# Optimization experiments

Measured on AMD Instinct MI355X. Metric: run time of the kernel, lower is better.

## Reference

```python
import jax, jax.numpy as jnp
import numpy as np

N_EMBD = 1024
N_HEADS = 16
HEAD_DIM = N_EMBD // N_HEADS


def setup_inputs() -> dict:
    key = jax.random.key(0)
    k0, k1, k2, k3, k4 = jax.random.split(key, 5)
    scale = 1.0 / np.sqrt(N_EMBD)
    x = jax.random.normal(k0, (2, 2048, N_EMBD), dtype=jnp.float32)
    # nn.Linear(n_embd, 3*n_embd): weight [3d, d], bias [3d]
    w_qkv = jax.random.normal(k1, (3 * N_EMBD, N_EMBD), dtype=jnp.float32) * scale
    b_qkv = jax.random.normal(k2, (3 * N_EMBD,), dtype=jnp.float32) * scale
    w_proj = jax.random.normal(k3, (N_EMBD, N_EMBD), dtype=jnp.float32) * scale
    b_proj = jax.random.normal(k4, (N_EMBD,), dtype=jnp.float32) * scale
    return {"x": x, "w_qkv": w_qkv, "b_qkv": b_qkv, "w_proj": w_proj, "b_proj": b_proj}


def reference(x, w_qkv, b_qkv, w_proj, b_proj):
    b, l, d = x.shape
    h, f = N_HEADS, HEAD_DIM
    qkv = x @ w_qkv.T + b_qkv                      # [b, l, 3d]
    # rearrange 'b l (c h f) -> c b h l f'
    qkv = qkv.reshape(b, l, 3, h, f)
    q = jnp.transpose(qkv[:, :, 0], (0, 2, 1, 3))  # [b, h, l, f]
    k = jnp.transpose(qkv[:, :, 1], (0, 2, 1, 3))
    v = jnp.transpose(qkv[:, :, 2], (0, 2, 1, 3))
    scores = jnp.einsum('bhqf,bhkf->bhqk', q, k) / jnp.sqrt(jnp.float32(f))
    att = jax.nn.softmax(scores, axis=-1)          # [b, h, l, l]
    y = jnp.einsum('bhqk,bhkf->bhqf', att, v)      # [b, h, l, f]
    y = jnp.transpose(y, (0, 2, 1, 3)).reshape(b, l, d)  # 'b h l f -> b l (h f)'
    return y @ w_proj.T + b_proj
```

## Files before the change

kernel.cpp:

```cpp
#include <hip/hip_runtime.h>
#include <hip/hip_bf16.h>
#include <stdint.h>


typedef unsigned short u16;
typedef __attribute__((ext_vector_type(8))) short short8;
typedef __attribute__((ext_vector_type(4))) float f32x4;
typedef __attribute__((ext_vector_type(16))) float f32x16;
typedef __attribute__((ext_vector_type(4))) unsigned int u32x4;

#define MFMA16(a, b, c) __builtin_amdgcn_mfma_f32_16x16x32_bf16((a), (b), (c), 0, 0, 0)
#define MFMA32(a, b, c) __builtin_amdgcn_mfma_f32_32x32x16_bf16((a), (b), (c), 0, 0, 0)

__device__ __forceinline__ u16 f2bf(float x) {
  union { float f; uint32_t u; } v; v.f = x;
  uint32_t r = v.u + 0x7FFFu + ((v.u >> 16) & 1u);
  return (u16)(r >> 16);
}

__device__ __forceinline__ float fexp2(float x) {
#if __has_builtin(__builtin_amdgcn_exp2f)
  return __builtin_amdgcn_exp2f(x);
#else
  return exp2f(x);
#endif
}

__device__ __forceinline__ uint32_t pkbf(float lo, float hi) {
  uint32_t a = __builtin_bit_cast(uint32_t, lo) + 0x8000u;
  uint32_t b = __builtin_bit_cast(uint32_t, hi) + 0x8000u;
  return __builtin_amdgcn_perm(b, a, 0x07060302u);
}

__device__ __forceinline__ void gload16(const void* g, void* l) {
  __builtin_amdgcn_global_load_lds((const __attribute__((address_space(1))) void*)g,
                                   (__attribute__((address_space(3))) void*)l, 16, 0, 0);
}

__global__ __launch_bounds__(256) void cvt_all(const float* __restrict__ x,
                                               const float* __restrict__ wq,
                                               const float* __restrict__ wp,
                                               u16* __restrict__ xb,
                                               u16* __restrict__ wqb,
                                               u16* __restrict__ wpb) {
  int i = blockIdx.x * 256 + threadIdx.x;
  const float* s; u16* d; int off;
  if (i < 1048576) { s = x; d = xb; off = i; }
  else if (i < 1835008) { s = wq; d = wqb; off = i - 1048576; }
  else { s = wp; d = wpb; off = i - 1835008; }
  float4 f = reinterpret_cast<const float4*>(s)[off];
  ushort4 o;
  o.x = f2bf(f.x); o.y = f2bf(f.y); o.z = f2bf(f.z); o.w = f2bf(f.w);
  reinterpret_cast<ushort4*>(d)[off] = o;
}

template <int EPI>
__global__ __launch_bounds__(256, 4) void gemm_bt(const u16* __restrict__ A,
                                                  const u16* __restrict__ B,
                                                  const float* __restrict__ bias,
                                                  u16* __restrict__ outb,
                                                  float* __restrict__ outf,
                                                  int M, int N, int K) {
  __shared__ u16 smem[16384];
  const int tid = threadIdx.x;
  const int lane = tid & 63;
  const int wid = tid >> 6;
  const int bn = blockIdx.x, bm = blockIdx.y;
  const int row0 = bm * 128, col0 = bn * 128;
  const int wr = wid >> 1, wc = wid & 1;
  const int fr = lane & 15, fq = lane >> 4;

  f32x4 acc[4][4];
  #pragma unroll
  for (int m = 0; m < 4; m++)
    #pragma unroll
    for (int n = 0; n < 4; n++)
      #pragma unroll
      for (int j = 0; j < 4; j++) acc[m][n][j] = 0.f;

  const int cB = tid + 256;
  const int rA1 = tid >> 2, rA2 = cB >> 2;
  const int lA1 = (tid & 3) ^ ((tid >> 3) & 3);
  const int lA2 = (cB & 3) ^ ((cB >> 3) & 3);
  const size_t ga1 = (size_t)rA1 * K + lA1 * 8;
  const size_t ga2 = (size_t)rA2 * K + lA2 * 8;
  const int d1 = tid * 8, d2 = cB * 8;
  const u16* Ab = A + (size_t)row0 * K;
  const u16* Bb = B + (size_t)col0 * K;

  const int sl = (fq ^ ((fr >> 1) & 3)) * 8;

  const int niter = K >> 5;

  {
    u16* s = smem;
    gload16(Ab + ga1, s + d1);
    gload16(Ab + ga2, s + d2);
    gload16(Bb + ga1, s + 4096 + d1);
    gload16(Bb + ga2, s + 4096 + d2);
  }
  __syncthreads();

  for (int t = 0; t < niter; t++) {
    if (t + 1 < niter) {
      u16* s = smem + ((t + 1) & 1) * 8192;
      const size_t k0 = (size_t)(t + 1) * 32;
      gload16(Ab + ga1 + k0, s + d1);
      gload16(Ab + ga2 + k0, s + d2);
      gload16(Bb + ga1 + k0, s + 4096 + d1);
      gload16(Bb + ga2 + k0, s + 4096 + d2);
    }
    const u16* sa = smem + (t & 1) * 8192;
    const u16* sb = sa + 4096;
    short8 a[4], b[4];
    #pragma unroll
    for (int m = 0; m < 4; m++)
      a[m] = *(const short8*)&sa[(wr * 64 + m * 16 + fr) * 32 + sl];
    #pragma unroll
    for (int n = 0; n < 4; n++)
      b[n] = *(const short8*)&sb[(wc * 64 + n * 16 + fr) * 32 + sl];
    __builtin_amdgcn_s_setprio(1);
    #pragma unroll
    for (int m = 0; m < 4; m++)
      #pragma unroll
      for (int n = 0; n < 4; n++)
        acc[m][n] = MFMA16(a[m], b[n], acc[m][n]);
    __builtin_amdgcn_s_setprio(0);
    __syncthreads();
  }

  if (EPI == 0) {
    if (bn < 16) {
      #pragma unroll
      for (int m = 0; m < 4; m++) {
        #pragma unroll
        for (int n = 0; n < 4; n++) {
          #pragma unroll
          for (int j = 0; j < 4; j++) {
            int r = row0 + wr * 64 + m * 16 + fq * 4 + j;
            int c = col0 + wc * 64 + n * 16 + fr;
            float v = acc[m][n][j] + bias[c];
            int d = c & 1023, h = d >> 6, f = d & 63;
            int bb = r >> 11, ll = r & 2047;
            int bhh = bb * 16 + h;
            if (bn < 8) {
              outb[((size_t)bhh * 2048 + ll) * 64 + f] = f2bf(v * 0.18033688f);
            } else {
              outb[4194304u + ((size_t)bhh * 2048 + ll) * 64 + f] = f2bf(v);
            }
          }
        }
      }
    } else {
      u16* sC = smem;
      #pragma unroll
      for (int m = 0; m < 4; m++) {
        #pragma unroll
        for (int n = 0; n < 4; n++) {
          int c_local = wc * 64 + n * 16 + fr;
          int r_base = wr * 64 + m * 16 + fq * 4;
          float bi = bias[col0 + c_local];
          uint2 w;
          w.x = pkbf(acc[m][n][0] + bi, acc[m][n][1] + bi);
          w.y = pkbf(acc[m][n][2] + bi, acc[m][n][3] + bi);
          *(uint2*)&sC[c_local * 128 + (r_base ^ ((c_local & 7) << 3))] = w;
        }
      }
      __syncthreads();
      const int h0 = (col0 - 2048) >> 6;
      const int ll0 = row0 & 2047;
      const int bb = row0 >> 11;
      #pragma unroll
      for (int it = 0; it < 8; it++) {
        int chunk = tid + it * 256;
        int row_c = chunk >> 4, off = chunk & 15;
        short8 v = *(const short8*)&sC[row_c * 128 + ((off * 8) ^ ((row_c & 7) << 3))];
        int h = h0 + (row_c >> 6), f = row_c & 63;
        *(short8*)&outb[8388608u + ((size_t)((bb * 16 + h) * 64 + f)) * 2048 + ll0 + off * 8] = v;
      }
    }
  } else {
    #pragma unroll
    for (int m = 0; m < 4; m++)
      #pragma unroll
      for (int n = 0; n < 4; n++)
        #pragma unroll
        for (int j = 0; j < 4; j++) {
          int r = row0 + wr * 64 + m * 16 + fq * 4 + j;
          int c = col0 + wc * 64 + n * 16 + fr;
          outf[(size_t)r * N + c] = acc[m][n][j] + bias[c];
        }
  }
}

__device__ __forceinline__ void softpack(const f32x16& st, float& lp,
                                         short8& paA, short8& paB) {
  float e[16];
  #pragma unroll
  for (int r = 0; r < 16; r++) e[r] = fexp2(st[r]);
  #pragma unroll
  for (int r = 0; r < 16; r++) lp += e[r];
  #pragma unroll
  for (int cc = 0; cc < 2; cc++) {
    uint32_t g0 = pkbf(e[8 * cc + 0], e[8 * cc + 1]);
    uint32_t g1 = pkbf(e[8 * cc + 2], e[8 * cc + 3]);
    uint32_t g2 = pkbf(e[8 * cc + 4], e[8 * cc + 5]);
    uint32_t g3 = pkbf(e[8 * cc + 6], e[8 * cc + 7]);
    asm volatile("v_permlane32_swap_b32 %0, %1" : "+v"(g0), "+v"(g2));
    asm volatile("v_permlane32_swap_b32 %0, %1" : "+v"(g1), "+v"(g3));
    u32x4 t;
    t[0] = g0; t[1] = g1; t[2] = g2; t[3] = g3;
    if (cc == 0) paA = __builtin_bit_cast(short8, t);
    else paB = __builtin_bit_cast(short8, t);
  }
}

__global__ __launch_bounds__(128, 2) void attn_kernel(const u16* __restrict__ qg,
                                                      const u16* __restrict__ kg,
                                                      const u16* __restrict__ vtg,
                                                      u16* __restrict__ y) {
  __shared__ u16 sK[2][4096];
  __shared__ u16 sVt[2][4096];
  __shared__ float sLv[2][32];
  const int x = blockIdx.x;
  const int bh = (x & 7) * 4 + (x >> 8);
  const int qt = (x >> 3) & 31;
  const int tid = threadIdx.x, l = tid & 63, wid = tid >> 6;
  const int col = l & 31, hi = l >> 5;
  const size_t base = (size_t)bh * 131072;
  const u16* qp = qg + base;
  const u16* kp = kg + base;
  const u16* vp = vtg + base;
  const int qrow = qt * 64 + wid * 32;

  short8 qf[4];
  #pragma unroll
  for (int kk = 0; kk < 4; kk++)
    qf[kk] = *(const short8*)&qp[(size_t)(qrow + col) * 64 + kk * 16 + hi * 8];

  int koff[4], voff[4], dst[4];
  #pragma unroll
  for (int j = 0; j < 4; j++) {
    int c = tid + j * 128;
    int row = c >> 3, slot = c & 7;
    int swc = (slot * 8) ^ ((row & 7) << 3);
    koff[j] = row * 64 + swc;
    voff[j] = row * 2048 + swc;
    dst[j] = c * 8;
  }

  f32x16 o0, o1;
  float lp = 0.f;
  #pragma unroll
  for (int r = 0; r < 16; r++) { o0[r] = 0.f; o1[r] = 0.f; }

  const int rsw = (col & 7) << 3;

  #pragma unroll
  for (int j = 0; j < 4; j++) {
    gload16(kp + koff[j], &sK[0][dst[j]]);
    gload16(vp + voff[j], &sVt[0][dst[j]]);
  }

  int sel = 0;
  for (int t0 = 0; t0 < 2048; t0 += 64) {
    __syncthreads();
    if (t0 + 64 < 2048) {
      const int tn = t0 + 64;
      #pragma unroll
      for (int j = 0; j < 4; j++) {
        gload16(kp + (size_t)tn * 64 + koff[j], &sK[sel ^ 1][dst[j]]);
        gload16(vp + tn + voff[j], &sVt[sel ^ 1][dst[j]]);
      }
    }
    const u16* Kt = sK[sel];
    const u16* Vt = sVt[sel];

    f32x16 st0, st1;
    #pragma unroll
    for (int r = 0; r < 16; r++) { st0[r] = 0.f; st1[r] = 0.f; }
    __builtin_amdgcn_s_setprio(1);
    #pragma unroll
    for (int kk = 0; kk < 4; kk++) {
      short8 kb0 = *(const short8*)&Kt[(col) * 64 + ((kk * 16 + hi * 8) ^ rsw)];
      short8 kb1 = *(const short8*)&Kt[(32 + col) * 64 + ((kk * 16 + hi * 8) ^ rsw)];
      st0 = MFMA32(kb0, qf[kk], st0);
      st1 = MFMA32(kb1, qf[kk], st1);
    }
    __builtin_amdgcn_s_setprio(0);

    short8 pa[4];
    softpack(st0, lp, pa[0], pa[1]);
    softpack(st1, lp, pa[2], pa[3]);

    __builtin_amdgcn_s_setprio(1);
    #pragma unroll
    for (int c = 0; c < 4; c++) {
      short8 vb0 = *(const short8*)&Vt[(col) * 64 + ((c * 16 + hi * 8) ^ rsw)];
      short8 vb1 = *(const short8*)&Vt[(32 + col) * 64 + ((c * 16 + hi * 8) ^ rsw)];
      o0 = MFMA32(pa[c], vb0, o0);
      o1 = MFMA32(pa[c], vb1, o1);
    }
    __builtin_amdgcn_s_setprio(0);
    sel ^= 1;
  }

  float lsum = lp + __shfl_xor(lp, 32);
  float linv = 1.0f / lsum;
  if (l < 32) sLv[wid][col] = linv;
  const int b = bh >> 4, hh = bh & 15;
  #pragma unroll
  for (int fvt = 0; fvt < 2; fvt++) {
    #pragma unroll
    for (int r = 0; r < 16; r++) {
      int q = (r & 3) + 8 * (r >> 2) + 4 * hi;
      float li = sLv[wid][q];
      float v = (fvt == 0 ? o0[r] : o1[r]) * li;
      y[((size_t)(b * 2048 + qrow + q)) * 1024 + hh * 64 + fvt * 32 + col] = f2bf(v);
    }
  }
}

extern "C" void kernel_launch(void* const* d_in, const int* in_sizes, int n_in,
                              void* d_out, int out_size, void* d_ws, size_t ws_size,
                              hipStream_t stream) {
  const float* x = (const float*)d_in[0];
  const float* w_qkv = (const float*)d_in[1];
  const float* b_qkv = (const float*)d_in[2];
  const float* w_proj = (const float*)d_in[3];
  const float* b_proj = (const float*)d_in[4];
  float* out = (float*)d_out;

  u16* ws = (u16*)d_ws;
  u16* xb = ws;
  u16* wq = xb + 4194304;
  u16* wp = wq + 3145728;
  u16* qb = wp + 1048576;
  u16* kb = qb + 4194304;
  u16* vb = kb + 4194304;
  u16* yb = vb + 4194304;

  cvt_all<<<8192, 256, 0, stream>>>(x, w_qkv, w_proj, xb, wq, wp);

  gemm_bt<0><<<dim3(24, 32), 256, 0, stream>>>(xb, wq, b_qkv, qb, nullptr, 4096, 3072, 1024);

  attn_kernel<<<1024, 128, 0, stream>>>(qb, kb, vb, yb);

  gemm_bt<1><<<dim3(8, 32), 256, 0, stream>>>(yb, wp, b_proj, nullptr, out, 4096, 1024, 1024);
}
```

Before: 121.2 us.

## Split attention key range across two wave pairs and merge partial outputs

The attention block grows from 2 to 4 waves. Each pair of waves handles half of the key/value sequence (split-K), with 32-key tiles staged per half. The partial outputs and row sums are then combined through shared memory before normalisation and the store. This raises parallelism and latency hiding per block, at the cost of a shared-memory reduction step and extra synchronisation. It relies on scores needing no max subtraction, same as the existing code.

Result: no change. 121.8 us (+0.4%).

```diff
diff --git a/kernel.cpp b/kernel.cpp
--- a/kernel.cpp
+++ b/kernel.cpp
@@ -89,7 +89,6 @@
   const u16* Bb = B + (size_t)col0 * K;
 
   const int sl = (fq ^ ((fr >> 1) & 3)) * 8;
-
   const int niter = K >> 5;
 
   {
@@ -193,8 +192,8 @@
   }
 }
 
-__device__ __forceinline__ void softpack(const f32x16& st, float& lp,
-                                         short8& paA, short8& paB) {
+__device__ __forceinline__ void softpack1(const f32x16& st, float& lp,
+                                          short8& paA, short8& paB) {
   float e[16];
   #pragma unroll
   for (int r = 0; r < 16; r++) e[r] = fexp2(st[r]);
@@ -215,89 +214,90 @@
   }
 }
 
-__global__ __launch_bounds__(128, 2) void attn_kernel(const u16* __restrict__ qg,
+__global__ __launch_bounds__(256, 4) void attn_kernel(const u16* __restrict__ qg,
                                                       const u16* __restrict__ kg,
                                                       const u16* __restrict__ vtg,
                                                       u16* __restrict__ y) {
-  __shared__ u16 sK[2][4096];
-  __shared__ u16 sVt[2][4096];
-  __shared__ float sLv[2][32];
+  __shared__ u16 sStage[16384];
+  __shared__ float sL2[64];
   const int x = blockIdx.x;
   const int bh = (x & 7) * 4 + (x >> 8);
   const int qt = (x >> 3) & 31;
   const int tid = threadIdx.x, l = tid & 63, wid = tid >> 6;
+  const int qs = wid & 1, kh = wid >> 1;
   const int col = l & 31, hi = l >> 5;
   const size_t base = (size_t)bh * 131072;
   const u16* qp = qg + base;
-  const u16* kp = kg + base;
-  const u16* vp = vtg + base;
-  const int qrow = qt * 64 + wid * 32;
+  const u16* kp = kg + base + (size_t)kh * 1024 * 64;
+  const u16* vp = vtg + base + (size_t)kh * 1024;
+  const int qrow = qt * 64 + qs * 32;
 
   short8 qf[4];
   #pragma unroll
   for (int kk = 0; kk < 4; kk++)
     qf[kk] = *(const short8*)&qp[(size_t)(qrow + col) * 64 + kk * 16 + hi * 8];
 
-  int koff[4], voff[4], dst[4];
-  #pragma unroll
-  for (int j = 0; j < 4; j++) {
-    int c = tid + j * 128;
-    int row = c >> 3, slot = c & 7;
-    int swc = (slot * 8) ^ ((row & 7) << 3);
-    koff[j] = row * 64 + swc;
-    voff[j] = row * 2048 + swc;
-    dst[j] = c * 8;
-  }
+  const int kc_row = tid >> 3;
+  const int kc_src = kc_row * 64 + (((tid & 7) ^ ((tid >> 3) & 7)) * 8);
+  const int vc_row = tid >> 2;
+  const int vc_src = vc_row * 2048 + (((tid & 3) ^ ((tid >> 3) & 3)) * 8);
+  const int kdst = tid * 8;
+  const int vdst = 2048 + tid * 8;
+  u16* S0 = sStage;
+  u16* S1 = sStage + 8192;
+  const u16* kp0 = kg + base;
+  const u16* kp1 = kg + base + 65536;
+  const u16* vp0 = vtg + base;
+  const u16* vp1 = vtg + base + 1024;
 
   f32x16 o0, o1;
   float lp = 0.f;
   #pragma unroll
   for (int r = 0; r < 16; r++) { o0[r] = 0.f; o1[r] = 0.f; }
 
-  const int rsw = (col & 7) << 3;
-
-  #pragma unroll
-  for (int j = 0; j < 4; j++) {
-    gload16(kp + koff[j], &sK[0][dst[j]]);
-    gload16(vp + voff[j], &sVt[0][dst[j]]);
-  }
-
+  const int krsw = (col & 7) << 3;
+  const int vrsw = ((col >> 1) & 3) << 3;
+
+  gload16(kp0 + kc_src, S0 + kdst);
+  gload16(vp0 + vc_src, S0 + vdst);
+  gload16(kp1 + kc_src, S1 + kdst);
+  gload16(vp1 + vc_src, S1 + vdst);
+
+  const u16* Sw = sStage + kh * 8192;
   int sel = 0;
-  for (int t0 = 0; t0 < 2048; t0 += 64) {
+  for (int t = 0; t < 32; t++) {
     __syncthreads();
-    if (t0 + 64 < 2048) {
-      const int tn = t0 + 64;
-      #pragma unroll
-      for (int j = 0; j < 4; j++) {
-        gload16(kp + (size_t)tn * 64 + koff[j], &sK[sel ^ 1][dst[j]]);
-        gload16(vp + tn + voff[j], &sVt[sel ^ 1][dst[j]]);
-      }
-    }
-    const u16* Kt = sK[sel];
-    const u16* Vt = sVt[sel];
-
-    f32x16 st0, st1;
-    #pragma unroll
-    for (int r = 0; r < 16; r++) { st0[r] = 0.f; st1[r] = 0.f; }
+    if (t + 1 < 32) {
+      const size_t ko = (size_t)(t + 1) * 32 * 64;
+      const int vo = (t + 1) * 32;
+      u16* b0 = S0 + (sel ^ 1) * 4096;
+      u16* b1 = S1 + (sel ^ 1) * 4096;
+      gload16(kp0 + ko + kc_src, b0 + kdst);
+      gload16(vp0 + vo + vc_src, b0 + vdst);
+      gload16(kp1 + ko + kc_src, b1 + kdst);
+      gload16(vp1 + vo + vc_src, b1 + vdst);
+    }
+    const u16* S = Sw + sel * 4096;
+
+    f32x16 st;
+    #pragma unroll
+    for (int r = 0; r < 16; r++) st[r] = 0.f;
     __builtin_amdgcn_s_setprio(1);
     #pragma unroll
     for (int kk = 0; kk < 4; kk++) {
-      short8 kb0 = *(const short8*)&Kt[(col) * 64 + ((kk * 16 + hi * 8) ^ rsw)];
-      short8 kb1 = *(const short8*)&Kt[(32 + col) * 64 + ((kk * 16 + hi * 8) ^ rsw)];
-      st0 = MFMA32(kb0, qf[kk], st0);
-      st1 = MFMA32(kb1, qf[kk], st1);
+      short8 kb = *(const short8*)&S[col * 64 + ((kk * 16 + hi * 8) ^ krsw)];
+      st = MFMA32(kb, qf[kk], st);
     }
     __builtin_amdgcn_s_setprio(0);
 
-    short8 pa[4];
-    softpack(st0, lp, pa[0], pa[1]);
-    softpack(st1, lp, pa[2], pa[3]);
+    short8 pa[2];
+    softpack1(st, lp, pa[0], pa[1]);
 
     __builtin_amdgcn_s_setprio(1);
     #pragma unroll
-    for (int c = 0; c < 4; c++) {
-      short8 vb0 = *(const short8*)&Vt[(col) * 64 + ((c * 16 + hi * 8) ^ rsw)];
-      short8 vb1 = *(const short8*)&Vt[(32 + col) * 64 + ((c * 16 + hi * 8) ^ rsw)];
+    for (int c = 0; c < 2; c++) {
+      short8 vb0 = *(const short8*)&S[2048 + col * 32 + ((c * 16 + hi * 8) ^ vrsw)];
+      short8 vb1 = *(const short8*)&S[2048 + (32 + col) * 32 + ((c * 16 + hi * 8) ^ vrsw)];
       o0 = MFMA32(pa[c], vb0, o0);
       o1 = MFMA32(pa[c], vb1, o1);
     }
@@ -305,18 +305,38 @@
     sel ^= 1;
   }
 
-  float lsum = lp + __shfl_xor(lp, 32);
-  float linv = 1.0f / lsum;
-  if (l < 32) sLv[wid][col] = linv;
-  const int b = bh >> 4, hh = bh & 15;
-  #pragma unroll
-  for (int fvt = 0; fvt < 2; fvt++) {
+  __syncthreads();
+  float* sM = (float*)sStage;
+  float* sMl = sM + 4096;
+  if (kh == 1) {
     #pragma unroll
     for (int r = 0; r < 16; r++) {
-      int q = (r & 3) + 8 * (r >> 2) + 4 * hi;
-      float li = sLv[wid][q];
-      float v = (fvt == 0 ? o0[r] : o1[r]) * li;
-      y[((size_t)(b * 2048 + qrow + q)) * 1024 + hh * 64 + fvt * 32 + col] = f2bf(v);
+      sM[qs * 2048 + r * 64 + l] = o0[r];
+      sM[qs * 2048 + (16 + r) * 64 + l] = o1[r];
+    }
+    sMl[qs * 64 + l] = lp;
+  }
+  __syncthreads();
+  if (kh == 0) {
+    #pragma unroll
+    for (int r = 0; r < 16; r++) {
+      o0[r] += sM[qs * 2048 + r * 64 + l];
+      o1[r] += sM[qs * 2048 + (16 + r) * 64 + l];
+    }
+    lp += sMl[qs * 64 + l];
+    float lsum = lp + __shfl_xor(lp, 32);
+    if (l < 32) sL2[qs * 32 + col] = 1.0f / lsum;
+    __builtin_amdgcn_s_waitcnt(0);
+    const int b = bh >> 4, hh = bh & 15;
+    #pragma unroll
+    for (int fvt = 0; fvt < 2; fvt++) {
+      #pragma unroll
+      for (int r = 0; r < 16; r++) {
+        int q = (r & 3) + 8 * (r >> 2) + 4 * hi;
+        float li = sL2[qs * 32 + q];
+        float v = (fvt == 0 ? o0[r] : o1[r]) * li;
+        y[((size_t)(b * 2048 + qrow + q)) * 1024 + hh * 64 + fvt * 32 + col] = f2bf(v);
+      }
     }
   }
 }
@@ -344,7 +364,7 @@
 
   gemm_bt<0><<<dim3(24, 32), 256, 0, stream>>>(xb, wq, b_qkv, qb, nullptr, 4096, 3072, 1024);
 
-  attn_kernel<<<1024, 128, 0, stream>>>(qb, kb, vb, yb);
+  attn_kernel<<<1024, 256, 0, stream>>>(qb, kb, vb, yb);
 
   gemm_bt<1><<<dim3(8, 32), 256, 0, stream>>>(yb, wp, b_proj, nullptr, out, 4096, 1024, 1024);
 }
```
